# Optimization experiments

Hardware: AMD Instinct MI355X
Metric: run time of the kernel (lower is better)

## Reference

```python
import jax, jax.numpy as jnp
import numpy as np

C = 512
HEADS = 8
HEAD_DIM = C // HEADS
GROUPS = 32
EPS = 1e-5
SCALE = HEAD_DIM ** -0.5


def setup_inputs() -> dict:
    key = jax.random.key(0)
    ks = jax.random.split(key, 6)
    b, h, w = 16, 32, 32
    x = jax.random.normal(ks[0], (b, C, h, w), dtype=jnp.float32)
    gn_gamma = jnp.ones((C,), dtype=jnp.float32)
    gn_beta = jnp.zeros((C,), dtype=jnp.float32)
    w_qkv = jax.random.normal(ks[1], (3 * C, C), dtype=jnp.float32) * (C ** -0.5)
    b_qkv = jax.random.normal(ks[2], (3 * C,), dtype=jnp.float32) * 0.01
    w_out = jax.random.normal(ks[3], (C, C), dtype=jnp.float32) * (C ** -0.5)
    b_out = jax.random.normal(ks[4], (C,), dtype=jnp.float32) * 0.01
    return {"x": x, "gn_gamma": gn_gamma, "gn_beta": gn_beta,
            "w_qkv": w_qkv, "b_qkv": b_qkv, "w_out": w_out, "b_out": b_out}


def reference(x, gn_gamma, gn_beta, w_qkv, b_qkv, w_out, b_out):
    b, c, h, w = x.shape
    hw = h * w
    # GroupNorm over (channels_per_group, H, W)
    xg = x.reshape(b, GROUPS, c // GROUPS, hw)
    mu = xg.mean(axis=(2, 3), keepdims=True)
    var = ((xg - mu) ** 2).mean(axis=(2, 3), keepdims=True)
    xn = ((xg - mu) * jax.lax.rsqrt(var + EPS)).reshape(b, c, h, w)
    xn = xn * gn_gamma[None, :, None, None] + gn_beta[None, :, None, None]
    # 1x1 conv QKV == channel matmul
    qkv = jnp.einsum('bchw,oc->bohw', xn, w_qkv) + b_qkv[None, :, None, None]
    q, k, v = jnp.split(qkv, 3, axis=1)
    q = q.reshape(b, HEADS, HEAD_DIM, hw)
    k = k.reshape(b, HEADS, HEAD_DIM, hw)
    v = v.reshape(b, HEADS, HEAD_DIM, hw)
    # attn[n,m] = <q[:,n], k[:,m]> * scale ; softmax over m (key positions)
    attn = jax.nn.softmax(jnp.einsum('bhdn,bhdm->bhnm', q, k) * SCALE, axis=-1)
    # out[d,n] = sum_m attn[n,m] * v[d,m]
    out = jnp.einsum('bhnm,bhdm->bhdn', attn, v).reshape(b, c, h, w)
    out = jnp.einsum('bchw,oc->bohw', out, w_out) + b_out[None, :, None, None]
    return out + x  # use_residual=True; dropout=0.0 is identity
```

## Files before the change

### kernel.cpp

```cpp
#include <hip/hip_runtime.h>
#include <math.h>

#define C_CH 512
#define HW   1024
#define GROUPS 32
#define CPG  16
#define EPS  1e-5f
#define HEADS 8
#define HD   64
#define SCALE 0.125f

typedef short bf16x8 __attribute__((ext_vector_type(8)));
typedef float f32x4  __attribute__((ext_vector_type(4)));
typedef unsigned short us8 __attribute__((ext_vector_type(8)));
typedef unsigned short us4 __attribute__((ext_vector_type(4)));

__device__ inline unsigned short f2bf(float x) {
  unsigned u = __float_as_uint(x);
  u += 0x7fffu + ((u >> 16) & 1u);
  return (unsigned short)(u >> 16);
}
__device__ inline float bf2f(unsigned short h) {
  return __uint_as_float(((unsigned)h) << 16);
}

__global__ __launch_bounds__(256) void wconv(const float* __restrict__ w,
    unsigned short* __restrict__ hi, unsigned short* __restrict__ lo, int n8) {
  const int i = blockIdx.x * 256 + threadIdx.x;
  if (i >= n8) return;
  const float4* w4 = (const float4*)w;
  const float4 a = w4[i * 2], b = w4[i * 2 + 1];
  const float v[8] = {a.x, a.y, a.z, a.w, b.x, b.y, b.z, b.w};
  us8 h, l;
#pragma unroll
  for (int j = 0; j < 8; ++j) {
    const unsigned short hb = f2bf(v[j]);
    h[j] = hb;
    l[j] = f2bf(v[j] - bf2f(hb));
  }
  *(us8*)(hi + (size_t)i * 8) = h;
  *(us8*)(lo + (size_t)i * 8) = l;
}

__global__ __launch_bounds__(256) void gn_t_kernel(
    const float* __restrict__ x, const float* __restrict__ gamma,
    const float* __restrict__ beta, unsigned short* __restrict__ xnt_hi,
    unsigned short* __restrict__ xnt_lo) {
  const int g = blockIdx.x;
  const int b = blockIdx.y;
  const int t = threadIdx.x;
  const size_t base = ((size_t)b * C_CH + (size_t)g * CPG) * HW;
  const float4* __restrict__ xin4 = (const float4*)(x + base);

  float s = 0.f, ss = 0.f;
  float4 v[16];
#pragma unroll
  for (int i = 0; i < 16; ++i) {
    float4 a = xin4[t + i * 256];
    v[i] = a;
    s  += a.x + a.y + a.z + a.w;
    ss += a.x * a.x + a.y * a.y + a.z * a.z + a.w * a.w;
  }
#pragma unroll
  for (int m = 32; m >= 1; m >>= 1) {
    s  += __shfl_xor(s, m);
    ss += __shfl_xor(ss, m);
  }
  __shared__ float red[8];
  const int wave = t >> 6;
  if ((t & 63) == 0) { red[wave * 2] = s; red[wave * 2 + 1] = ss; }
  __syncthreads();
  s  = red[0] + red[2] + red[4] + red[6];
  ss = red[1] + red[3] + red[5] + red[7];
  const float mean = s * (1.f / 16384.f);
  const float var  = ss * (1.f / 16384.f) - mean * mean;
  const float inv  = rsqrtf(var + EPS);

  float gms[16], bts[16];
#pragma unroll
  for (int i = 0; i < 16; ++i) {
    gms[i] = gamma[g * CPG + i] * inv;
    bts[i] = beta[g * CPG + i];
  }

#pragma unroll
  for (int c = 0; c < 4; ++c) {
    unsigned short hh[16], ll[16];
#pragma unroll
    for (int i = 0; i < 16; ++i) {
      const float xv = (c == 0) ? v[i].x : (c == 1) ? v[i].y : (c == 2) ? v[i].z : v[i].w;
      const float y = (xv - mean) * gms[i] + bts[i];
      const unsigned short hb = f2bf(y);
      hh[i] = hb;
      ll[i] = f2bf(y - bf2f(hb));
    }
    const size_t off = ((size_t)b * HW + 4 * t + c) * C_CH + g * CPG;
    us8 H0, H1, L0, L1;
#pragma unroll
    for (int j = 0; j < 8; ++j) { H0[j] = hh[j]; H1[j] = hh[j + 8]; L0[j] = ll[j]; L1[j] = ll[j + 8]; }
    *(us8*)(xnt_hi + off)     = H0;
    *(us8*)(xnt_hi + off + 8) = H1;
    *(us8*)(xnt_lo + off)     = L0;
    *(us8*)(xnt_lo + off + 8) = L1;
  }
}

__global__ __launch_bounds__(256) void t_conv(const float* __restrict__ in,
    unsigned short* __restrict__ hi, unsigned short* __restrict__ lo) {
  const int c0 = blockIdx.x * 64;
  const int h0 = blockIdx.y * 64;
  const int b  = blockIdx.z;
  __shared__ float s[64][68];
  const int t = threadIdx.x;
  const float* ip = in + (size_t)b * C_CH * HW;
#pragma unroll
  for (int r = 0; r < 4; ++r) {
    const int f4 = r * 256 + t;
    const int rc = f4 >> 4, c4 = f4 & 15;
    const float4 a = *(const float4*)(ip + (size_t)(c0 + rc) * HW + h0 + c4 * 4);
    s[rc][c4 * 4 + 0] = a.x; s[rc][c4 * 4 + 1] = a.y;
    s[rc][c4 * 4 + 2] = a.z; s[rc][c4 * 4 + 3] = a.w;
  }
  __syncthreads();
  unsigned short* hp = hi + (size_t)b * HW * C_CH;
  unsigned short* lp = lo + (size_t)b * HW * C_CH;
#pragma unroll
  for (int r = 0; r < 4; ++r) {
    const int u = r * 256 + t;
    const int hw = u >> 4, c4 = u & 15;
    us4 H, L;
#pragma unroll
    for (int j = 0; j < 4; ++j) {
      const float xv = s[c4 * 4 + j][hw];
      const unsigned short hb = f2bf(xv);
      H[j] = hb;
      L[j] = f2bf(xv - bf2f(hb));
    }
    const size_t off = (size_t)(h0 + hw) * C_CH + c0 + c4 * 4;
    *(us4*)(hp + off) = H;
    *(us4*)(lp + off) = L;
  }
}

__global__ __launch_bounds__(256, 2) void gemm_bt_split(
    const unsigned short* __restrict__ Ah, const unsigned short* __restrict__ Al,
    const unsigned short* __restrict__ Bh0, const unsigned short* __restrict__ Bl0,
    const float* __restrict__ bias, const float* __restrict__ R0,
    float* __restrict__ C0, int M) {
  const int n0 = blockIdx.x * 128;
  const int m0 = blockIdx.y * 128;
  const int b  = blockIdx.z;
  const unsigned short* __restrict__ Bh = Bh0 + (size_t)b * HW * C_CH;
  const unsigned short* __restrict__ Bl = Bl0 + (size_t)b * HW * C_CH;
  float* __restrict__ Cp = C0 + (size_t)b * M * HW;
  const float* __restrict__ Rp = R0 ? (R0 + (size_t)b * M * HW) : nullptr;

  __shared__ unsigned short sAh[128 * 64], sAl[128 * 64], sBh[128 * 64], sBl[128 * 64];

  const int t  = threadIdx.x;
  const int l  = t & 63, w = t >> 6;
  const int wm = w >> 1, wn = w & 1;
  const int ln = l & 15, lg = l >> 4;

  f32x4 acc[4][4];
#pragma unroll
  for (int i = 0; i < 4; ++i)
#pragma unroll
    for (int j = 0; j < 4; ++j) acc[i][j] = (f32x4){0.f, 0.f, 0.f, 0.f};

  for (int k0 = 0; k0 < C_CH; k0 += 64) {
    __syncthreads();
#pragma unroll
    for (int rr = 0; rr < 4; ++rr) {
      const int flat = rr * 256 + t;
      const int row = flat >> 3, ch = flat & 7;
      const int dst = row * 64 + (ch ^ (row & 7)) * 8;
      const size_t asrc = (size_t)(m0 + row) * C_CH + k0 + ch * 8;
      const size_t bsrc = (size_t)(n0 + row) * C_CH + k0 + ch * 8;
      *(bf16x8*)&sAh[dst] = *(const bf16x8*)(Ah + asrc);
      *(bf16x8*)&sAl[dst] = *(const bf16x8*)(Al + asrc);
      *(bf16x8*)&sBh[dst] = *(const bf16x8*)(Bh + bsrc);
      *(bf16x8*)&sBl[dst] = *(const bf16x8*)(Bl + bsrc);
    }
    __syncthreads();
#pragma unroll
    for (int ks = 0; ks < 2; ++ks) {
      bf16x8 bhf[4], blf[4];
#pragma unroll
      for (int fn = 0; fn < 4; ++fn) {
        const int row = wn * 64 + fn * 16 + ln;
        const int off = row * 64 + ((ks * 4 + lg) ^ (row & 7)) * 8;
        bhf[fn] = *(const bf16x8*)&sBh[off];
        blf[fn] = *(const bf16x8*)&sBl[off];
      }
#pragma unroll
      for (int fm = 0; fm < 4; ++fm) {
        const int row = wm * 64 + fm * 16 + ln;
        const int off = row * 64 + ((ks * 4 + lg) ^ (row & 7)) * 8;
        const bf16x8 ahf = *(const bf16x8*)&sAh[off];
        const bf16x8 alf = *(const bf16x8*)&sAl[off];
#pragma unroll
        for (int fn = 0; fn < 4; ++fn) {
          acc[fm][fn] = __builtin_amdgcn_mfma_f32_16x16x32_bf16(ahf, bhf[fn], acc[fm][fn], 0, 0, 0);
          acc[fm][fn] = __builtin_amdgcn_mfma_f32_16x16x32_bf16(ahf, blf[fn], acc[fm][fn], 0, 0, 0);
          acc[fm][fn] = __builtin_amdgcn_mfma_f32_16x16x32_bf16(alf, bhf[fn], acc[fm][fn], 0, 0, 0);
        }
      }
    }
  }
#pragma unroll
  for (int fm = 0; fm < 4; ++fm) {
#pragma unroll
    for (int r = 0; r < 4; ++r) {
      const int row = m0 + wm * 64 + fm * 16 + lg * 4 + r;
      const float bi = bias[row];
#pragma unroll
      for (int fn = 0; fn < 4; ++fn) {
        const int col = n0 + wn * 64 + fn * 16 + ln;
        const size_t off = (size_t)row * HW + col;
        float vo = acc[fm][fn][r] + bi;
        if (Rp) vo += Rp[off];
        Cp[off] = vo;
      }
    }
  }
}

__global__ __launch_bounds__(256) void attn_kernel(
    const float* __restrict__ qkv, float* __restrict__ out) {
  const int qb = blockIdx.x;
  const int h  = blockIdx.y;
  const int b  = blockIdx.z;
  const int t  = threadIdx.x;
  const int tx = t & 15, ty = t >> 4;

  __shared__ float Qs[64 * 64];
  __shared__ float Ks[64 * 64];
  __shared__ float Vs[64 * 64];
  __shared__ float Ps[64 * 64];

  const size_t bh = ((size_t)b * 3 * C_CH + (size_t)h * HD) * HW;
  const float* __restrict__ qp = qkv + bh;
  const float* __restrict__ kp = qkv + bh + (size_t)C_CH * HW;
  const float* __restrict__ vp = qkv + bh + (size_t)2 * C_CH * HW;
  const int n0 = qb * 64;

#pragma unroll
  for (int li = 0; li < 16; ++li) {
    const int flat = li * 256 + t;
    const int d = flat >> 6, n = flat & 63;
    Qs[flat] = qp[(size_t)d * HW + n0 + n] * SCALE;
  }

  float m_run[4], l_run[4], acc[4][4] = {};
#pragma unroll
  for (int i = 0; i < 4; ++i) { m_run[i] = -INFINITY; l_run[i] = 0.f; }

  for (int mt = 0; mt < 16; ++mt) {
    const int mbase = mt * 64;
    __syncthreads();
#pragma unroll
    for (int li = 0; li < 16; ++li) {
      const int flat = li * 256 + t;
      const int d = flat >> 6, m = flat & 63;
      Ks[flat] = kp[(size_t)d * HW + mbase + m];
      Vs[m * 64 + (d ^ (m & 28))] = vp[(size_t)d * HW + mbase + m];
    }
    __syncthreads();

    float s[4][4] = {};
#pragma unroll 8
    for (int d = 0; d < 64; ++d) {
      const float4 q4 = *(const float4*)&Qs[d * 64 + ty * 4];
      const float4 k4 = *(const float4*)&Ks[d * 64 + tx * 4];
      const float av[4] = {q4.x, q4.y, q4.z, q4.w};
      const float bv[4] = {k4.x, k4.y, k4.z, k4.w};
#pragma unroll
      for (int i = 0; i < 4; ++i)
#pragma unroll
        for (int j = 0; j < 4; ++j)
          s[i][j] = fmaf(av[i], bv[j], s[i][j]);
    }

#pragma unroll
    for (int i = 0; i < 4; ++i) {
      float tm = fmaxf(fmaxf(s[i][0], s[i][1]), fmaxf(s[i][2], s[i][3]));
#pragma unroll
      for (int m = 8; m >= 1; m >>= 1) tm = fmaxf(tm, __shfl_xor(tm, m));
      const float mn = fmaxf(m_run[i], tm);
      const float al = __expf(m_run[i] - mn);
      float rs = 0.f;
#pragma unroll
      for (int j = 0; j < 4; ++j) {
        const float p = __expf(s[i][j] - mn);
        s[i][j] = p;
        rs += p;
      }
#pragma unroll
      for (int m = 8; m >= 1; m >>= 1) rs += __shfl_xor(rs, m);
      l_run[i] = l_run[i] * al + rs;
      m_run[i] = mn;
#pragma unroll
      for (int j = 0; j < 4; ++j) acc[i][j] *= al;
#pragma unroll
      for (int j = 0; j < 4; ++j) Ps[(ty * 4 + i) * 64 + tx * 4 + j] = s[i][j];
    }
    __syncthreads();

#pragma unroll 4
    for (int m = 0; m < 64; ++m) {
      const float4 v4 = *(const float4*)&Vs[m * 64 + ((tx * 4) ^ (m & 28))];
      const float vv[4] = {v4.x, v4.y, v4.z, v4.w};
#pragma unroll
      for (int i = 0; i < 4; ++i) {
        const float p = Ps[(ty * 4 + i) * 64 + m];
#pragma unroll
        for (int j = 0; j < 4; ++j)
          acc[i][j] = fmaf(p, vv[j], acc[i][j]);
      }
    }
  }

  __syncthreads();
#pragma unroll
  for (int i = 0; i < 4; ++i) {
    const float invl = 1.f / l_run[i];
    const int n = 4 * ty + i;
#pragma unroll
    for (int j = 0; j < 4; ++j) {
      const int d = 4 * tx + j;
      Ps[n * 64 + (d ^ (n & 31))] = acc[i][j] * invl;
    }
  }
  __syncthreads();
  float* __restrict__ op = out + ((size_t)b * C_CH + (size_t)h * HD) * HW + n0;
#pragma unroll
  for (int li = 0; li < 16; ++li) {
    const int flat = li * 256 + t;
    const int d = flat >> 6, n = flat & 63;
    op[(size_t)d * HW + n] = Ps[n * 64 + (d ^ (n & 31))];
  }
}

extern "C" void kernel_launch(void* const* d_in, const int* in_sizes, int n_in,
                              void* d_out, int out_size, void* d_ws, size_t ws_size,
                              hipStream_t stream) {
  (void)in_sizes; (void)n_in; (void)out_size; (void)ws_size;
  const float* x     = (const float*)d_in[0];
  const float* gamma = (const float*)d_in[1];
  const float* beta  = (const float*)d_in[2];
  const float* w_qkv = (const float*)d_in[3];
  const float* b_qkv = (const float*)d_in[4];
  const float* w_out = (const float*)d_in[5];
  const float* b_out = (const float*)d_in[6];
  float* out = (float*)d_out;

  unsigned short* xnt_hi = (unsigned short*)d_ws;
  unsigned short* xnt_lo = xnt_hi + (size_t)16 * HW * C_CH;
  float* qkv   = (float*)((char*)d_ws + (size_t)32 * 1024 * 1024);
  float* attno = (float*)d_ws;
  unsigned short* att_hi = (unsigned short*)((char*)d_ws + (size_t)32 * 1024 * 1024);
  unsigned short* att_lo = att_hi + (size_t)16 * HW * C_CH;
  unsigned short* wo_hi  = (unsigned short*)((char*)d_ws + (size_t)64 * 1024 * 1024);
  unsigned short* wo_lo  = wo_hi + 512 * 512;
  unsigned short* wq_hi = (unsigned short*)d_out;
  unsigned short* wq_lo = wq_hi + (size_t)1536 * 512;

  wconv<<<dim3(384), 256, 0, stream>>>(w_qkv, wq_hi, wq_lo, 98304);
  gn_t_kernel<<<dim3(GROUPS, 16), 256, 0, stream>>>(x, gamma, beta, xnt_hi, xnt_lo);
  gemm_bt_split<<<dim3(8, 12, 16), 256, 0, stream>>>(wq_hi, wq_lo, xnt_hi, xnt_lo,
                                                     b_qkv, nullptr, qkv, 3 * C_CH);
  attn_kernel<<<dim3(16, HEADS, 16), 256, 0, stream>>>(qkv, attno);
  t_conv<<<dim3(8, 16, 16), 256, 0, stream>>>(attno, att_hi, att_lo);
  wconv<<<dim3(128), 256, 0, stream>>>(w_out, wo_hi, wo_lo, 32768);
  gemm_bt_split<<<dim3(8, 4, 16), 256, 0, stream>>>(wo_hi, wo_lo, att_hi, att_lo,
                                                    b_out, x, out, C_CH);
}
```

Baseline: 819.9 us.

## Move attention to split-bf16 MFMA with position-major QKV layout

Replaces the scalar-FMA fp32 flash-attention kernel with an MFMA version that uses hi/lo bf16 splitting (three MFMAs per product) for both QK^T and PV. The QKV GEMM now writes position-major hi/lo bf16 Q/K and V directly, a small transpose kernel produces a d-major V, and the attention output is emitted as hi/lo bf16 in the layout the output GEMM consumes, which removes the separate t_conv pass. The aim is to cut attention compute time and fp32 intermediate traffic. The trade-off is more workspace buffers and reading K/V straight from global memory with no LDS staging.

```diff
diff --git a/kernel.cpp b/kernel.cpp
--- a/kernel.cpp
+++ b/kernel.cpp
@@ -13,7 +13,6 @@
 typedef short bf16x8 __attribute__((ext_vector_type(8)));
 typedef float f32x4  __attribute__((ext_vector_type(4)));
 typedef unsigned short us8 __attribute__((ext_vector_type(8)));
-typedef unsigned short us4 __attribute__((ext_vector_type(4)));
 
 __device__ inline unsigned short f2bf(float x) {
   unsigned u = __float_as_uint(x);
@@ -82,7 +81,6 @@
     gms[i] = gamma[g * CPG + i] * inv;
     bts[i] = beta[g * CPG + i];
   }
-
 #pragma unroll
   for (int c = 0; c < 4; ++c) {
     unsigned short hh[16], ll[16];
@@ -105,40 +103,255 @@
   }
 }
 
-__global__ __launch_bounds__(256) void t_conv(const float* __restrict__ in,
-    unsigned short* __restrict__ hi, unsigned short* __restrict__ lo) {
-  const int c0 = blockIdx.x * 64;
-  const int h0 = blockIdx.y * 64;
-  const int b  = blockIdx.z;
-  __shared__ float s[64][68];
-  const int t = threadIdx.x;
-  const float* ip = in + (size_t)b * C_CH * HW;
-#pragma unroll
-  for (int r = 0; r < 4; ++r) {
-    const int f4 = r * 256 + t;
-    const int rc = f4 >> 4, c4 = f4 & 15;
-    const float4 a = *(const float4*)(ip + (size_t)(c0 + rc) * HW + h0 + c4 * 4);
-    s[rc][c4 * 4 + 0] = a.x; s[rc][c4 * 4 + 1] = a.y;
-    s[rc][c4 * 4 + 2] = a.z; s[rc][c4 * 4 + 3] = a.w;
+__global__ __launch_bounds__(256, 2) void gemm_xw(
+    const unsigned short* __restrict__ Ah0, const unsigned short* __restrict__ Al0,
+    const unsigned short* __restrict__ Bh, const unsigned short* __restrict__ Bl,
+    const float* __restrict__ bias,
+    unsigned short* __restrict__ qk_hi, unsigned short* __restrict__ qk_lo,
+    unsigned short* __restrict__ vb_hi, unsigned short* __restrict__ vb_lo) {
+  const int n0 = blockIdx.x * 128;
+  const int m0 = blockIdx.y * 128;
+  const int bz = blockIdx.z;
+  const unsigned short* __restrict__ Ah = Ah0 + (size_t)bz * HW * C_CH;
+  const unsigned short* __restrict__ Al = Al0 + (size_t)bz * HW * C_CH;
+
+  __shared__ unsigned short sAh[128 * 64], sAl[128 * 64], sBh[128 * 64], sBl[128 * 64];
+
+  const int t  = threadIdx.x;
+  const int l  = t & 63, w = t >> 6;
+  const int wm = w >> 1, wn = w & 1;
+  const int ln = l & 15, lg = l >> 4;
+
+  f32x4 acc[4][4];
+#pragma unroll
+  for (int i = 0; i < 4; ++i)
+#pragma unroll
+    for (int j = 0; j < 4; ++j) acc[i][j] = (f32x4){0.f, 0.f, 0.f, 0.f};
+
+  for (int k0 = 0; k0 < C_CH; k0 += 64) {
+    __syncthreads();
+#pragma unroll
+    for (int rr = 0; rr < 4; ++rr) {
+      const int flat = rr * 256 + t;
+      const int row = flat >> 3, ch = flat & 7;
+      const int dst = row * 64 + (ch ^ (row & 7)) * 8;
+      const size_t asrc = (size_t)(m0 + row) * C_CH + k0 + ch * 8;
+      const size_t bsrc = (size_t)(n0 + row) * C_CH + k0 + ch * 8;
+      *(bf16x8*)&sAh[dst] = *(const bf16x8*)(Ah + asrc);
+      *(bf16x8*)&sAl[dst] = *(const bf16x8*)(Al + asrc);
+      *(bf16x8*)&sBh[dst] = *(const bf16x8*)(Bh + bsrc);
+      *(bf16x8*)&sBl[dst] = *(const bf16x8*)(Bl + bsrc);
+    }
+    __syncthreads();
+#pragma unroll
+    for (int ks = 0; ks < 2; ++ks) {
+      bf16x8 bhf[4], blf[4];
+#pragma unroll
+      for (int fn = 0; fn < 4; ++fn) {
+        const int row = wn * 64 + fn * 16 + ln;
+        const int off = row * 64 + ((ks * 4 + lg) ^ (row & 7)) * 8;
+        bhf[fn] = *(const bf16x8*)&sBh[off];
+        blf[fn] = *(const bf16x8*)&sBl[off];
+      }
+#pragma unroll
+      for (int fm = 0; fm < 4; ++fm) {
+        const int row = wm * 64 + fm * 16 + ln;
+        const int off = row * 64 + ((ks * 4 + lg) ^ (row & 7)) * 8;
+        const bf16x8 ahf = *(const bf16x8*)&sAh[off];
+        const bf16x8 alf = *(const bf16x8*)&sAl[off];
+#pragma unroll
+        for (int fn = 0; fn < 4; ++fn) {
+          acc[fm][fn] = __builtin_amdgcn_mfma_f32_16x16x32_bf16(ahf, bhf[fn], acc[fm][fn], 0, 0, 0);
+          acc[fm][fn] = __builtin_amdgcn_mfma_f32_16x16x32_bf16(ahf, blf[fn], acc[fm][fn], 0, 0, 0);
+          acc[fm][fn] = __builtin_amdgcn_mfma_f32_16x16x32_bf16(alf, bhf[fn], acc[fm][fn], 0, 0, 0);
+        }
+      }
+    }
+  }
+  const int isv = (n0 >= 1024);
+  unsigned short* __restrict__ dh = isv ? vb_hi : qk_hi;
+  unsigned short* __restrict__ dl = isv ? vb_lo : qk_lo;
+  const int ldo = isv ? 512 : 1024;
+  const int cb  = isv ? 1024 : 0;
+#pragma unroll
+  for (int fm = 0; fm < 4; ++fm) {
+#pragma unroll
+    for (int r = 0; r < 4; ++r) {
+      const int row = m0 + wm * 64 + fm * 16 + lg * 4 + r;
+      const size_t rb = ((size_t)bz * 1024 + row) * ldo;
+#pragma unroll
+      for (int fn = 0; fn < 4; ++fn) {
+        const int col = n0 + wn * 64 + fn * 16 + ln;
+        const float v = acc[fm][fn][r] + bias[col];
+        const unsigned short hb = f2bf(v);
+        const size_t o = rb + (col - cb);
+        dh[o] = hb;
+        dl[o] = f2bf(v - bf2f(hb));
+      }
+    }
+  }
+}
+
+__global__ __launch_bounds__(256) void vt_kernel(
+    const unsigned short* __restrict__ vb_hi, const unsigned short* __restrict__ vb_lo,
+    unsigned short* __restrict__ vt_hi, unsigned short* __restrict__ vt_lo) {
+  const int hw0 = blockIdx.x * 64;
+  const int h   = blockIdx.y;
+  const int b   = blockIdx.z;
+  const int t   = threadIdx.x;
+  __shared__ unsigned T[64][64];
+#pragma unroll
+  for (int it = 0; it < 2; ++it) {
+    const int flat = it * 256 + t;
+    const int hwl = flat >> 3, c = flat & 7;
+    const size_t src = ((size_t)b * 1024 + hw0 + hwl) * 512 + h * 64 + c * 8;
+    const us8 H = *(const us8*)(vb_hi + src);
+    const us8 L = *(const us8*)(vb_lo + src);
+#pragma unroll
+    for (int j = 0; j < 8; ++j) {
+      const int d = c * 8 + j;
+      T[hwl][d ^ (hwl & 31)] = (unsigned)H[j] | ((unsigned)L[j] << 16);
+    }
   }
   __syncthreads();
-  unsigned short* hp = hi + (size_t)b * HW * C_CH;
-  unsigned short* lp = lo + (size_t)b * HW * C_CH;
-#pragma unroll
-  for (int r = 0; r < 4; ++r) {
-    const int u = r * 256 + t;
-    const int hw = u >> 4, c4 = u & 15;
-    us4 H, L;
-#pragma unroll
-    for (int j = 0; j < 4; ++j) {
-      const float xv = s[c4 * 4 + j][hw];
-      const unsigned short hb = f2bf(xv);
-      H[j] = hb;
-      L[j] = f2bf(xv - bf2f(hb));
-    }
-    const size_t off = (size_t)(h0 + hw) * C_CH + c0 + c4 * 4;
-    *(us4*)(hp + off) = H;
-    *(us4*)(lp + off) = L;
+#pragma unroll
+  for (int it = 0; it < 2; ++it) {
+    const int flat = it * 256 + t;
+    const int dl = flat >> 3, hc = flat & 7;
+    us8 H2, L2;
+#pragma unroll
+    for (int j = 0; j < 8; ++j) {
+      const int hwl = hc * 8 + j;
+      const unsigned u = T[hwl][dl ^ (hwl & 31)];
+      H2[j] = (unsigned short)(u & 0xffffu);
+      L2[j] = (unsigned short)(u >> 16);
+    }
+    const size_t dst = ((size_t)b * 512 + h * 64 + dl) * 1024 + hw0 + hc * 8;
+    *(us8*)(vt_hi + dst) = H2;
+    *(us8*)(vt_lo + dst) = L2;
+  }
+}
+
+__global__ __launch_bounds__(256) void attn_mfma(
+    const unsigned short* __restrict__ qk_hi, const unsigned short* __restrict__ qk_lo,
+    const unsigned short* __restrict__ vt_hi, const unsigned short* __restrict__ vt_lo,
+    unsigned short* __restrict__ att_hi, unsigned short* __restrict__ att_lo) {
+  const int flatb = blockIdx.x + 16 * blockIdx.y + 128 * blockIdx.z;
+  const int hb = (flatb % 8) + 8 * ((flatb / 8) / 16);
+  const int qb = (flatb / 8) % 16;
+  const int h = hb % 8, b = hb / 8;
+
+  const int t  = threadIdx.x;
+  const int l  = t & 63, ws = t >> 6;
+  const int ln = l & 15, lg = l >> 4;
+
+  __shared__ unsigned short Ph[4][16 * 64];
+  __shared__ unsigned short Pl[4][16 * 64];
+
+  const size_t qkbase = (size_t)b * 1024 * 1024;
+  const int qrow = qb * 64 + ws * 16 + ln;
+  const size_t qoff = qkbase + (size_t)qrow * 1024 + h * 64;
+
+  bf16x8 q_h[2], q_l[2];
+#pragma unroll
+  for (int ks = 0; ks < 2; ++ks) {
+    q_h[ks] = *(const bf16x8*)(qk_hi + qoff + ks * 32 + lg * 8);
+    q_l[ks] = *(const bf16x8*)(qk_lo + qoff + ks * 32 + lg * 8);
+  }
+
+  float m_run[4], l_run[4];
+  f32x4 acc_o[4];
+#pragma unroll
+  for (int r = 0; r < 4; ++r) { m_run[r] = -INFINITY; l_run[r] = 0.f; }
+#pragma unroll
+  for (int fd = 0; fd < 4; ++fd) acc_o[fd] = (f32x4){0.f, 0.f, 0.f, 0.f};
+
+  const int kcol = 512 + h * 64;
+  const size_t vbase = ((size_t)b * 512 + h * 64) * 1024;
+
+  for (int mt = 0; mt < 16; ++mt) {
+    const int mb = mt * 64;
+    f32x4 acc_s[4];
+#pragma unroll
+    for (int fn = 0; fn < 4; ++fn) acc_s[fn] = (f32x4){0.f, 0.f, 0.f, 0.f};
+#pragma unroll
+    for (int ks = 0; ks < 2; ++ks) {
+#pragma unroll
+      for (int fn = 0; fn < 4; ++fn) {
+        const size_t koff = qkbase + (size_t)(mb + fn * 16 + ln) * 1024 + kcol + ks * 32 + lg * 8;
+        const bf16x8 kh = *(const bf16x8*)(qk_hi + koff);
+        const bf16x8 kl = *(const bf16x8*)(qk_lo + koff);
+        acc_s[fn] = __builtin_amdgcn_mfma_f32_16x16x32_bf16(q_h[ks], kh, acc_s[fn], 0, 0, 0);
+        acc_s[fn] = __builtin_amdgcn_mfma_f32_16x16x32_bf16(q_h[ks], kl, acc_s[fn], 0, 0, 0);
+        acc_s[fn] = __builtin_amdgcn_mfma_f32_16x16x32_bf16(q_l[ks], kh, acc_s[fn], 0, 0, 0);
+      }
+    }
+    float al[4];
+#pragma unroll
+    for (int r = 0; r < 4; ++r) {
+      float s0 = acc_s[0][r] * SCALE, s1 = acc_s[1][r] * SCALE;
+      float s2 = acc_s[2][r] * SCALE, s3 = acc_s[3][r] * SCALE;
+      float tm = fmaxf(fmaxf(s0, s1), fmaxf(s2, s3));
+#pragma unroll
+      for (int msk = 8; msk >= 1; msk >>= 1) tm = fmaxf(tm, __shfl_xor(tm, msk));
+      const float mn = fmaxf(m_run[r], tm);
+      al[r] = __expf(m_run[r] - mn);
+      m_run[r] = mn;
+      const float p0 = __expf(s0 - mn), p1 = __expf(s1 - mn);
+      const float p2 = __expf(s2 - mn), p3 = __expf(s3 - mn);
+      float rs = p0 + p1 + p2 + p3;
+#pragma unroll
+      for (int msk = 8; msk >= 1; msk >>= 1) rs += __shfl_xor(rs, msk);
+      l_run[r] = l_run[r] * al[r] + rs;
+      const int n = 4 * lg + r;
+      const int sw = (n >> 1) & 7;
+      const float pv4[4] = {p0, p1, p2, p3};
+#pragma unroll
+      for (int fn = 0; fn < 4; ++fn) {
+        const int m = fn * 16 + ln;
+        const unsigned short hb = f2bf(pv4[fn]);
+        const int idx = n * 64 + ((m >> 3) ^ sw) * 8 + (m & 7);
+        Ph[ws][idx] = hb;
+        Pl[ws][idx] = f2bf(pv4[fn] - bf2f(hb));
+      }
+    }
+#pragma unroll
+    for (int fd = 0; fd < 4; ++fd) {
+      f32x4 a = acc_o[fd];
+      a[0] *= al[0]; a[1] *= al[1]; a[2] *= al[2]; a[3] *= al[3];
+      acc_o[fd] = a;
+    }
+#pragma unroll
+    for (int ks = 0; ks < 2; ++ks) {
+      const int pc = ((ks * 4 + lg) ^ ((ln >> 1) & 7)) * 8;
+      const bf16x8 pah = *(const bf16x8*)&Ph[ws][ln * 64 + pc];
+      const bf16x8 pal = *(const bf16x8*)&Pl[ws][ln * 64 + pc];
+#pragma unroll
+      for (int fd = 0; fd < 4; ++fd) {
+        const size_t voff = vbase + (size_t)(fd * 16 + ln) * 1024 + mb + ks * 32 + lg * 8;
+        const bf16x8 vh = *(const bf16x8*)(vt_hi + voff);
+        const bf16x8 vl = *(const bf16x8*)(vt_lo + voff);
+        acc_o[fd] = __builtin_amdgcn_mfma_f32_16x16x32_bf16(pah, vh, acc_o[fd], 0, 0, 0);
+        acc_o[fd] = __builtin_amdgcn_mfma_f32_16x16x32_bf16(pah, vl, acc_o[fd], 0, 0, 0);
+        acc_o[fd] = __builtin_amdgcn_mfma_f32_16x16x32_bf16(pal, vh, acc_o[fd], 0, 0, 0);
+      }
+    }
+  }
+  float inv[4];
+#pragma unroll
+  for (int r = 0; r < 4; ++r) inv[r] = 1.f / l_run[r];
+#pragma unroll
+  for (int fd = 0; fd < 4; ++fd) {
+#pragma unroll
+    for (int r = 0; r < 4; ++r) {
+      const int row = qb * 64 + ws * 16 + 4 * lg + r;
+      const int col = h * 64 + fd * 16 + ln;
+      const float v = acc_o[fd][r] * inv[r];
+      const unsigned short hb = f2bf(v);
+      const size_t off = ((size_t)b * 1024 + row) * 512 + col;
+      att_hi[off] = hb;
+      att_lo[off] = f2bf(v - bf2f(hb));
+    }
   }
 }
 
@@ -226,122 +439,6 @@
   }
 }
 
-__global__ __launch_bounds__(256) void attn_kernel(
-    const float* __restrict__ qkv, float* __restrict__ out) {
-  const int qb = blockIdx.x;
-  const int h  = blockIdx.y;
-  const int b  = blockIdx.z;
-  const int t  = threadIdx.x;
-  const int tx = t & 15, ty = t >> 4;
-
-  __shared__ float Qs[64 * 64];
-  __shared__ float Ks[64 * 64];
-  __shared__ float Vs[64 * 64];
-  __shared__ float Ps[64 * 64];
-
-  const size_t bh = ((size_t)b * 3 * C_CH + (size_t)h * HD) * HW;
-  const float* __restrict__ qp = qkv + bh;
-  const float* __restrict__ kp = qkv + bh + (size_t)C_CH * HW;
-  const float* __restrict__ vp = qkv + bh + (size_t)2 * C_CH * HW;
-  const int n0 = qb * 64;
-
-#pragma unroll
-  for (int li = 0; li < 16; ++li) {
-    const int flat = li * 256 + t;
-    const int d = flat >> 6, n = flat & 63;
-    Qs[flat] = qp[(size_t)d * HW + n0 + n] * SCALE;
-  }
-
-  float m_run[4], l_run[4], acc[4][4] = {};
-#pragma unroll
-  for (int i = 0; i < 4; ++i) { m_run[i] = -INFINITY; l_run[i] = 0.f; }
-
-  for (int mt = 0; mt < 16; ++mt) {
-    const int mbase = mt * 64;
-    __syncthreads();
-#pragma unroll
-    for (int li = 0; li < 16; ++li) {
-      const int flat = li * 256 + t;
-      const int d = flat >> 6, m = flat & 63;
-      Ks[flat] = kp[(size_t)d * HW + mbase + m];
-      Vs[m * 64 + (d ^ (m & 28))] = vp[(size_t)d * HW + mbase + m];
-    }
-    __syncthreads();
-
-    float s[4][4] = {};
-#pragma unroll 8
-    for (int d = 0; d < 64; ++d) {
-      const float4 q4 = *(const float4*)&Qs[d * 64 + ty * 4];
-      const float4 k4 = *(const float4*)&Ks[d * 64 + tx * 4];
-      const float av[4] = {q4.x, q4.y, q4.z, q4.w};
-      const float bv[4] = {k4.x, k4.y, k4.z, k4.w};
-#pragma unroll
-      for (int i = 0; i < 4; ++i)
-#pragma unroll
-        for (int j = 0; j < 4; ++j)
-          s[i][j] = fmaf(av[i], bv[j], s[i][j]);
-    }
-
-#pragma unroll
-    for (int i = 0; i < 4; ++i) {
-      float tm = fmaxf(fmaxf(s[i][0], s[i][1]), fmaxf(s[i][2], s[i][3]));
-#pragma unroll
-      for (int m = 8; m >= 1; m >>= 1) tm = fmaxf(tm, __shfl_xor(tm, m));
-      const float mn = fmaxf(m_run[i], tm);
-      const float al = __expf(m_run[i] - mn);
-      float rs = 0.f;
-#pragma unroll
-      for (int j = 0; j < 4; ++j) {
-        const float p = __expf(s[i][j] - mn);
-        s[i][j] = p;
-        rs += p;
-      }
-#pragma unroll
-      for (int m = 8; m >= 1; m >>= 1) rs += __shfl_xor(rs, m);
-      l_run[i] = l_run[i] * al + rs;
-      m_run[i] = mn;
-#pragma unroll
-      for (int j = 0; j < 4; ++j) acc[i][j] *= al;
-#pragma unroll
-      for (int j = 0; j < 4; ++j) Ps[(ty * 4 + i) * 64 + tx * 4 + j] = s[i][j];
-    }
-    __syncthreads();
-
-#pragma unroll 4
-    for (int m = 0; m < 64; ++m) {
-      const float4 v4 = *(const float4*)&Vs[m * 64 + ((tx * 4) ^ (m & 28))];
-      const float vv[4] = {v4.x, v4.y, v4.z, v4.w};
-#pragma unroll
-      for (int i = 0; i < 4; ++i) {
-        const float p = Ps[(ty * 4 + i) * 64 + m];
-#pragma unroll
-        for (int j = 0; j < 4; ++j)
-          acc[i][j] = fmaf(p, vv[j], acc[i][j]);
-      }
-    }
-  }
-
-  __syncthreads();
-#pragma unroll
-  for (int i = 0; i < 4; ++i) {
-    const float invl = 1.f / l_run[i];
-    const int n = 4 * ty + i;
-#pragma unroll
-    for (int j = 0; j < 4; ++j) {
-      const int d = 4 * tx + j;
-      Ps[n * 64 + (d ^ (n & 31))] = acc[i][j] * invl;
-    }
-  }
-  __syncthreads();
-  float* __restrict__ op = out + ((size_t)b * C_CH + (size_t)h * HD) * HW + n0;
-#pragma unroll
-  for (int li = 0; li < 16; ++li) {
-    const int flat = li * 256 + t;
-    const int d = flat >> 6, n = flat & 63;
-    op[(size_t)d * HW + n] = Ps[n * 64 + (d ^ (n & 31))];
-  }
-}
-
 extern "C" void kernel_launch(void* const* d_in, const int* in_sizes, int n_in,
                               void* d_out, int out_size, void* d_ws, size_t ws_size,
                               hipStream_t stream) {
@@ -355,23 +452,28 @@
   const float* b_out = (const float*)d_in[6];
   float* out = (float*)d_out;
 
-  unsigned short* xnt_hi = (unsigned short*)d_ws;
-  unsigned short* xnt_lo = xnt_hi + (size_t)16 * HW * C_CH;
-  float* qkv   = (float*)((char*)d_ws + (size_t)32 * 1024 * 1024);
-  float* attno = (float*)d_ws;
-  unsigned short* att_hi = (unsigned short*)((char*)d_ws + (size_t)32 * 1024 * 1024);
-  unsigned short* att_lo = att_hi + (size_t)16 * HW * C_CH;
-  unsigned short* wo_hi  = (unsigned short*)((char*)d_ws + (size_t)64 * 1024 * 1024);
-  unsigned short* wo_lo  = wo_hi + 512 * 512;
-  unsigned short* wq_hi = (unsigned short*)d_out;
-  unsigned short* wq_lo = wq_hi + (size_t)1536 * 512;
+  char* wsb = (char*)d_ws;
+  unsigned short* xnt_hi = (unsigned short*)wsb;
+  unsigned short* xnt_lo = (unsigned short*)(wsb + (size_t)16 * 1024 * 1024);
+  unsigned short* qk_hi  = (unsigned short*)(wsb + (size_t)32 * 1024 * 1024);
+  unsigned short* qk_lo  = (unsigned short*)(wsb + (size_t)64 * 1024 * 1024);
+  unsigned short* vb_hi  = (unsigned short*)(wsb + (size_t)96 * 1024 * 1024);
+  unsigned short* vb_lo  = (unsigned short*)(wsb + (size_t)112 * 1024 * 1024);
+  unsigned short* vt_hi  = xnt_hi;
+  unsigned short* vt_lo  = xnt_lo;
+  unsigned short* att_hi = vb_hi;
+  unsigned short* att_lo = vb_lo;
+  unsigned short* wo_hi  = qk_hi;
+  unsigned short* wo_lo  = qk_hi + 512 * 512;
+  unsigned short* wq_hi  = (unsigned short*)d_out;
+  unsigned short* wq_lo  = wq_hi + (size_t)1536 * 512;
 
   wconv<<<dim3(384), 256, 0, stream>>>(w_qkv, wq_hi, wq_lo, 98304);
   gn_t_kernel<<<dim3(GROUPS, 16), 256, 0, stream>>>(x, gamma, beta, xnt_hi, xnt_lo);
-  gemm_bt_split<<<dim3(8, 12, 16), 256, 0, stream>>>(wq_hi, wq_lo, xnt_hi, xnt_lo,
-                                                     b_qkv, nullptr, qkv, 3 * C_CH);
-  attn_kernel<<<dim3(16, HEADS, 16), 256, 0, stream>>>(qkv, attno);
-  t_conv<<<dim3(8, 16, 16), 256, 0, stream>>>(attno, att_hi, att_lo);
+  gemm_xw<<<dim3(12, 8, 16), 256, 0, stream>>>(xnt_hi, xnt_lo, wq_hi, wq_lo, b_qkv,
+                                               qk_hi, qk_lo, vb_hi, vb_lo);
+  vt_kernel<<<dim3(16, 8, 16), 256, 0, stream>>>(vb_hi, vb_lo, vt_hi, vt_lo);
+  attn_mfma<<<dim3(16, 8, 16), 256, 0, stream>>>(qk_hi, qk_lo, vt_hi, vt_lo, att_hi, att_lo);
   wconv<<<dim3(128), 256, 0, stream>>>(w_out, wo_hi, wo_lo, 32768);
   gemm_bt_split<<<dim3(8, 4, 16), 256, 0, stream>>>(wo_hi, wo_lo, att_hi, att_lo,
                                                     b_out, x, out, C_CH);
```

New measurement: 697.1 us. -15.0%, faster.
